# Kernel optimization log

Measured on AMD Instinct MI355X. Metric: run time of the kernel, lower is better.

Reference implementation:

```python
import jax, jax.numpy as jnp
import numpy as np

B, N, D_IN, D_OUT = 8, 2048, 1024, 1024


def setup_inputs() -> dict:
    key = jax.random.key(0)
    k0, k1, k2, k3 = jax.random.split(key, 4)
    scale = 1.0 / np.sqrt(D_IN)
    x = jax.random.normal(k0, (B, N, D_IN), dtype=jnp.float32)
    Wq = jax.random.normal(k1, (D_IN, D_OUT), dtype=jnp.float32) * scale
    Wk = jax.random.normal(k2, (D_IN, D_OUT), dtype=jnp.float32) * scale
    Wv = jax.random.normal(k3, (D_IN, D_OUT), dtype=jnp.float32) * scale
    return {"x": x, "Wq": Wq, "Wk": Wk, "Wv": Wv}


def reference(x, Wq, Wk, Wv):
    # x: [b, n, d_in]; single-head causal attention, dropout p=0 (eval).
    q = jnp.einsum('bnd,de->bne', x, Wq)
    k = jnp.einsum('bnd,de->bne', x, Wk)
    v = jnp.einsum('bnd,de->bne', x, Wv)
    n = x.shape[1]
    scores = jnp.einsum('bqe,bke->bqk', q, k)  # [b, n, n]
    causal_mask = jnp.triu(jnp.ones((n, n), dtype=bool), k=1)
    scores = jnp.where(causal_mask, -jnp.inf, scores)
    scale = 1.0 / jnp.sqrt(jnp.asarray(k.shape[-1], dtype=scores.dtype))
    attn = jax.nn.softmax(scores * scale, axis=-1)
    context = jnp.einsum('bqk,bke->bqe', attn, v)
    return context
```

## Files before the change

kernel.cpp:

```cpp
#include <hip/hip_runtime.h>


typedef unsigned short u16;
typedef __bf16 bf16x8 __attribute__((ext_vector_type(8)));
typedef float f32x4 __attribute__((ext_vector_type(4)));
typedef unsigned short u16x8 __attribute__((ext_vector_type(8)));
typedef unsigned short u16x4 __attribute__((ext_vector_type(4)));

static constexpr int BATCH = 8;
static constexpr int SEQ = 2048;
static constexpr int DIM = 1024;

static constexpr size_t SZ_XB = (size_t)BATCH * SEQ * DIM * 2;
static constexpr size_t SZ_W  = (size_t)DIM * DIM * 2;
static constexpr size_t OFF_XB  = 0;
static constexpr size_t OFF_WQT = OFF_XB + SZ_XB;
static constexpr size_t OFF_WKT = OFF_WQT + SZ_W;
static constexpr size_t OFF_WVT = OFF_WKT + SZ_W;
static constexpr size_t OFF_Q   = OFF_WVT + SZ_W;
static constexpr size_t OFF_K   = OFF_Q + SZ_XB;
static constexpr size_t OFF_VT  = OFF_K + SZ_XB;
static constexpr size_t OFF_E   = OFF_VT + SZ_XB;

__device__ __forceinline__ u16 f2b(float f) {
  unsigned u = __builtin_bit_cast(unsigned, f);
  u += 0x7fffu + ((u >> 16) & 1u);
  return (u16)(u >> 16);
}

__device__ __forceinline__ void gload16(const u16* g, u16* l) {
  __builtin_amdgcn_global_load_lds((__attribute__((address_space(1))) void*)g,
                                   (__attribute__((address_space(3))) void*)l, 16, 0, 0);
}

#define VWAIT(N) asm volatile("s_waitcnt vmcnt(" #N ")" ::: "memory")

__device__ __forceinline__ void barrier_raw() {
  __builtin_amdgcn_sched_barrier(0);
  __builtin_amdgcn_s_barrier();
  __builtin_amdgcn_sched_barrier(0);
}

__global__ __launch_bounds__(256) void cast_f32_bf16(const float* __restrict__ in,
                                                     u16* __restrict__ out) {
  const size_t i = ((size_t)blockIdx.x * 256 + threadIdx.x) * 8;
  float4 a = *(const float4*)(in + i);
  float4 b = *(const float4*)(in + i + 4);
  u16x8 o;
  o[0] = f2b(a.x); o[1] = f2b(a.y); o[2] = f2b(a.z); o[3] = f2b(a.w);
  o[4] = f2b(b.x); o[5] = f2b(b.y); o[6] = f2b(b.z); o[7] = f2b(b.w);
  *reinterpret_cast<u16x8*>(out + i) = o;
}

__global__ __launch_bounds__(256) void transpose_cast_w(const float* __restrict__ W,
                                                        u16* __restrict__ WT) {
  __shared__ float t[32][33];
  const int k0 = blockIdx.x * 32, n0 = blockIdx.y * 32;
  const int tx = threadIdx.x, ty = threadIdx.y;
#pragma unroll
  for (int dy = 0; dy < 32; dy += 8)
    t[ty + dy][tx] = W[(size_t)(k0 + ty + dy) * DIM + n0 + tx];
  __syncthreads();
#pragma unroll
  for (int dy = 0; dy < 32; dy += 8)
    WT[(size_t)(n0 + ty + dy) * DIM + k0 + tx] = f2b(t[tx][ty + dy]);
}

template <int MODE>
__global__ __launch_bounds__(512, 2) void gemm256(
    const u16* __restrict__ A, size_t sA, int lda,
    const u16* __restrict__ Bt, size_t sB, int ldb,
    void* __restrict__ C, size_t sC, int ldc,
    int Kdim, float scale) {
  const int bx = blockIdx.x, by = blockIdx.y, bz = blockIdx.z;
  if (MODE == 2 && bx > by) return;
  const u16* Ab = A + (size_t)bz * sA;
  const u16* Bb = Bt + (size_t)bz * sB;
  const int rowTile = by * 256, colTile = bx * 256;
  const int NT = Kdim >> 5;

  __shared__ __align__(16) u16 lds[4 * 16384];

  const int tid = threadIdx.x;
  const int w = tid >> 6, l = tid & 63;
  const int wm = w >> 2, wn = w & 3;
  const int lr = l & 15, quad = l >> 4;

  auto srow = [](int c) { int u = (c & 7) ^ ((c >> 3) & 7); return 2 * (c >> 3) + (u >> 2); };
  auto skq  = [](int c) { int u = (c & 7) ^ ((c >> 3) & 7); return u & 3; };
  const u16* pA0 = Ab + (size_t)(rowTile + srow(tid)) * lda + skq(tid) * 8;
  const u16* pA1 = Ab + (size_t)(rowTile + srow(tid + 512)) * lda + skq(tid + 512) * 8;
  const u16* pB0 = Bb + (size_t)(colTile + srow(tid)) * ldb + skq(tid) * 8;
  const u16* pB1 = Bb + (size_t)(colTile + srow(tid + 512)) * ldb + skq(tid + 512) * 8;

  int offA[8], offB[4];
#pragma unroll
  for (int mi = 0; mi < 8; ++mi) {
    const int row = wm * 128 + mi * 16 + lr;
    offA[mi] = ((row * 64 + quad * 16) ^ (((row >> 1) & 7) << 4)) >> 1;
  }
#pragma unroll
  for (int ni = 0; ni < 4; ++ni) {
    const int row = wn * 64 + ni * 16 + lr;
    offB[ni] = ((row * 64 + quad * 16) ^ (((row >> 1) & 7) << 4)) >> 1;
  }

  f32x4 acc[8][4];
#pragma unroll
  for (int i = 0; i < 8; ++i)
#pragma unroll
    for (int j = 0; j < 4; ++j) acc[i][j] = (f32x4){0.f, 0.f, 0.f, 0.f};

#define STAGE256(tt)                              \
  {                                               \
    u16* sb = &lds[((tt) & 3) * 16384];           \
    const int ko = (tt) * 32;                     \
    gload16(pA0 + ko, sb + w * 512);              \
    gload16(pA1 + ko, sb + 4096 + w * 512);       \
    gload16(pB0 + ko, sb + 8192 + w * 512);       \
    gload16(pB1 + ko, sb + 12288 + w * 512);      \
  }

  STAGE256(0);
  STAGE256(1);
  STAGE256(2);

  for (int t = 0; t < NT; ++t) {
    const u16* As = &lds[(t & 3) * 16384];
    const u16* Bs = As + 8192;
    if (t + 3 < NT) {
      STAGE256(t + 3);
      VWAIT(12);
    } else if (t + 2 < NT) {
      VWAIT(8);
    } else if (t + 1 < NT) {
      VWAIT(4);
    } else {
      VWAIT(0);
    }
    barrier_raw();
    bf16x8 af[8], bf[4];
#pragma unroll
    for (int mi = 0; mi < 8; ++mi)
      af[mi] = *reinterpret_cast<const bf16x8*>(&As[offA[mi]]);
#pragma unroll
    for (int ni = 0; ni < 4; ++ni)
      bf[ni] = *reinterpret_cast<const bf16x8*>(&Bs[offB[ni]]);
    __builtin_amdgcn_s_setprio(1);
#pragma unroll
    for (int mi = 0; mi < 8; ++mi)
#pragma unroll
      for (int ni = 0; ni < 4; ++ni)
        acc[mi][ni] =
            __builtin_amdgcn_mfma_f32_16x16x32_bf16(af[mi], bf[ni], acc[mi][ni], 0, 0, 0);
    __builtin_amdgcn_s_setprio(0);
    asm volatile("s_waitcnt lgkmcnt(0)" ::: "memory");
    barrier_raw();
  }
#undef STAGE256

  const int orow0 = rowTile + wm * 128 + quad * 4;
  const int ocol0 = colTile + wn * 64 + lr;
#pragma unroll
  for (int mi = 0; mi < 8; ++mi) {
#pragma unroll
    for (int ni = 0; ni < 4; ++ni) {
      const int colg = ocol0 + ni * 16;
      if (MODE == 1) {
        const int rowg0 = orow0 + mi * 16;
        const int bb = rowg0 >> 11, nn = rowg0 & (SEQ - 1);
        u16x4 pk;
#pragma unroll
        for (int r = 0; r < 4; ++r) pk[r] = f2b(acc[mi][ni][r]);
        *reinterpret_cast<u16x4*>(&((u16*)C)[(size_t)bb * sC + (size_t)colg * ldc + nn]) = pk;
      } else {
#pragma unroll
        for (int r = 0; r < 4; ++r) {
          const int rowg = orow0 + mi * 16 + r;
          const float v = acc[mi][ni][r];
          if (MODE == 0) {
            ((u16*)C)[(size_t)bz * sC + (size_t)rowg * ldc + colg] = f2b(v);
          } else {
            const float e = (colg <= rowg) ? __expf(v * scale) : 0.f;
            ((u16*)C)[(size_t)bz * sC + (size_t)rowg * ldc + colg] = f2b(e);
          }
        }
      }
    }
  }
}

template <int MODE>
__global__ __launch_bounds__(256, 2) void gemm_bt(
    const u16* __restrict__ A, size_t sA, int lda,
    const u16* __restrict__ Bt, size_t sB, int ldb,
    void* __restrict__ C, size_t sC, int ldc,
    int Kdim, float scale) {
  const int bx = blockIdx.x, bz = blockIdx.z;
  const int by = (MODE == 3) ? (int)(gridDim.y - 1 - blockIdx.y) : (int)blockIdx.y;
  if (MODE == 2 && bx > by) return;
  const u16* Ab = A + (size_t)bz * sA;
  const u16* Bb = Bt + (size_t)bz * sB;
  const int rowTile = by * 128, colTile = bx * 128;
  int kmax = Kdim;
  if (MODE == 3) {
    int km = (by + 1) * 128;
    if (km < kmax) kmax = km;
  }

  __shared__ __align__(16) u16 As[128 * 32];
  __shared__ __align__(16) u16 Bs[128 * 32];

  const int tid = threadIdx.x;
  const int w = tid >> 6, l = tid & 63;
  const int wr = (w >> 1) * 64, wc = (w & 1) * 64;
  const int lr = l & 15, quad = l >> 4;

  f32x4 acc[4][4];
#pragma unroll
  for (int i = 0; i < 4; ++i)
#pragma unroll
    for (int j = 0; j < 4; ++j) acc[i][j] = (f32x4){0.f, 0.f, 0.f, 0.f};
  float rsum[4] = {0.f, 0.f, 0.f, 0.f};

  const int srow = w * 16 + (l >> 2);
  const int scol = (l & 3) * 8;
  const u16* gA0 = Ab + (size_t)(rowTile + srow) * lda + scol;
  const u16* gA1 = gA0 + (size_t)64 * lda;
  const u16* gB0 = Bb + (size_t)(colTile + srow) * ldb + scol;
  const u16* gB1 = gB0 + (size_t)64 * ldb;
  u16* lA0 = &As[(w * 16) * 32];
  u16* lA1 = &As[(64 + w * 16) * 32];
  u16* lB0 = &Bs[(w * 16) * 32];
  u16* lB1 = &Bs[(64 + w * 16) * 32];

  for (int k0 = 0; k0 < kmax; k0 += 32) {
    __syncthreads();
    gload16(gA0 + k0, lA0);
    gload16(gA1 + k0, lA1);
    gload16(gB0 + k0, lB0);
    gload16(gB1 + k0, lB1);
    __syncthreads();
    bf16x8 af[4], bfr[4];
#pragma unroll
    for (int mi = 0; mi < 4; ++mi)
      af[mi] = *reinterpret_cast<const bf16x8*>(&As[(wr + mi * 16 + lr) * 32 + quad * 8]);
#pragma unroll
    for (int ni = 0; ni < 4; ++ni)
      bfr[ni] = *reinterpret_cast<const bf16x8*>(&Bs[(wc + ni * 16 + lr) * 32 + quad * 8]);
    if (MODE == 3) {
#pragma unroll
      for (int mi = 0; mi < 4; ++mi) {
        float s = 0.f;
#pragma unroll
        for (int j = 0; j < 8; ++j) s += (float)af[mi][j];
        rsum[mi] += s;
      }
    }
#pragma unroll
    for (int mi = 0; mi < 4; ++mi)
#pragma unroll
      for (int ni = 0; ni < 4; ++ni)
        acc[mi][ni] =
            __builtin_amdgcn_mfma_f32_16x16x32_bf16(af[mi], bfr[ni], acc[mi][ni], 0, 0, 0);
  }

  if (MODE == 3) {
#pragma unroll
    for (int mi = 0; mi < 4; ++mi) {
      rsum[mi] += __shfl_xor(rsum[mi], 16);
      rsum[mi] += __shfl_xor(rsum[mi], 32);
    }
  }

  const int orow0 = rowTile + wr + quad * 4;
  const int ocol0 = colTile + wc + lr;
#pragma unroll
  for (int mi = 0; mi < 4; ++mi) {
    float linv[4];
    if (MODE == 3) {
#pragma unroll
      for (int r = 0; r < 4; ++r) linv[r] = 1.f / __shfl(rsum[mi], quad * 4 + r);
    }
#pragma unroll
    for (int ni = 0; ni < 4; ++ni) {
      const int colg = ocol0 + ni * 16;
#pragma unroll
      for (int r = 0; r < 4; ++r) {
        const int rowg = orow0 + mi * 16 + r;
        const float v = acc[mi][ni][r];
        if (MODE == 0) {
          ((u16*)C)[(size_t)bz * sC + (size_t)rowg * ldc + colg] = f2b(v);
        } else if (MODE == 1) {
          const int bb = rowg >> 11, nn = rowg & (SEQ - 1);
          ((u16*)C)[(size_t)bb * sC + (size_t)colg * ldc + nn] = f2b(v);
        } else if (MODE == 2) {
          const float e = (colg <= rowg) ? __expf(v * scale) : 0.f;
          ((u16*)C)[(size_t)bz * sC + (size_t)rowg * ldc + colg] = f2b(e);
        } else {
          ((float*)C)[(size_t)bz * sC + (size_t)rowg * ldc + colg] = v * linv[r];
        }
      }
    }
  }
}

extern "C" void kernel_launch(void* const* d_in, const int* in_sizes, int n_in,
                              void* d_out, int out_size, void* d_ws, size_t ws_size,
                              hipStream_t stream) {
  const float* x = (const float*)d_in[0];
  const float* Wq = (const float*)d_in[1];
  const float* Wk = (const float*)d_in[2];
  const float* Wv = (const float*)d_in[3];
  float* out = (float*)d_out;
  char* ws = (char*)d_ws;

  u16* xb = (u16*)(ws + OFF_XB);
  u16* wqT = (u16*)(ws + OFF_WQT);
  u16* wkT = (u16*)(ws + OFF_WKT);
  u16* wvT = (u16*)(ws + OFF_WVT);
  u16* qb = (u16*)(ws + OFF_Q);
  u16* kb = (u16*)(ws + OFF_K);
  u16* vt = (u16*)(ws + OFF_VT);
  u16* eb = (u16*)(ws + OFF_E);

  const int total = BATCH * SEQ * DIM;
  cast_f32_bf16<<<total / (256 * 8), 256, 0, stream>>>(x, xb);
  transpose_cast_w<<<dim3(32, 32), dim3(32, 8), 0, stream>>>(Wq, wqT);
  transpose_cast_w<<<dim3(32, 32), dim3(32, 8), 0, stream>>>(Wk, wkT);
  transpose_cast_w<<<dim3(32, 32), dim3(32, 8), 0, stream>>>(Wv, wvT);

  gemm256<0><<<dim3(4, 64, 1), 512, 0, stream>>>(xb, 0, DIM, wqT, 0, DIM, qb, 0, DIM,
                                                 DIM, 1.f);
  gemm256<0><<<dim3(4, 64, 1), 512, 0, stream>>>(xb, 0, DIM, wkT, 0, DIM, kb, 0, DIM,
                                                 DIM, 1.f);
  gemm256<1><<<dim3(4, 64, 1), 512, 0, stream>>>(xb, 0, DIM, wvT, 0, DIM, vt,
                                                 (size_t)DIM * SEQ, SEQ, DIM, 1.f);
  gemm256<2><<<dim3(8, 8, BATCH), 512, 0, stream>>>(
      qb, (size_t)SEQ * DIM, DIM, kb, (size_t)SEQ * DIM, DIM, eb, (size_t)SEQ * SEQ, SEQ,
      DIM, 0.03125f);
  gemm_bt<3><<<dim3(8, 16, BATCH), 256, 0, stream>>>(
      eb, (size_t)SEQ * SEQ, SEQ, vt, (size_t)DIM * SEQ, SEQ, out, (size_t)SEQ * DIM, DIM,
      SEQ, 1.f);
}
```

Baseline: 417.4 us.

## Run PV GEMM on 256-tile pipelined kernel and split main loop into half-steps

Removes the simple 128-tile gemm_bt kernel. The attention-times-V GEMM now runs through the 256x256 four-stage LDS-pipelined kernel, with causal K truncation, row-sum accumulation and normalization added to it. The main loop is also restructured for all modes: B and A tile loads are issued separately, and the MFMA work is split into two halves so the LDS reads and next-stage loads for the second half overlap the first half's compute. The goal is better latency hiding and data reuse in the largest GEMM. The cost is more barriers per iteration, and bigger tiles leave fewer blocks with coarser causal work balance.

```diff
diff --git a/kernel.cpp b/kernel.cpp
--- a/kernel.cpp
+++ b/kernel.cpp
@@ -72,12 +72,18 @@
     const u16* __restrict__ Bt, size_t sB, int ldb,
     void* __restrict__ C, size_t sC, int ldc,
     int Kdim, float scale) {
-  const int bx = blockIdx.x, by = blockIdx.y, bz = blockIdx.z;
+  const int bx = blockIdx.x, bz = blockIdx.z;
+  const int by = (MODE == 3) ? (int)(gridDim.y - 1 - blockIdx.y) : (int)blockIdx.y;
   if (MODE == 2 && bx > by) return;
   const u16* Ab = A + (size_t)bz * sA;
   const u16* Bb = Bt + (size_t)bz * sB;
   const int rowTile = by * 256, colTile = bx * 256;
-  const int NT = Kdim >> 5;
+  int kmax = Kdim;
+  if (MODE == 3) {
+    int km = (by + 1) * 256;
+    if (km < kmax) kmax = km;
+  }
+  const int NT = kmax >> 5;
 
   __shared__ __align__(16) u16 lds[4 * 16384];
 
@@ -110,59 +116,110 @@
   for (int i = 0; i < 8; ++i)
 #pragma unroll
     for (int j = 0; j < 4; ++j) acc[i][j] = (f32x4){0.f, 0.f, 0.f, 0.f};
-
-#define STAGE256(tt)                              \
+  float rsum[8] = {0.f, 0.f, 0.f, 0.f, 0.f, 0.f, 0.f, 0.f};
+
+#define STAGE_B(tt)                               \
+  {                                               \
+    u16* sb = &lds[((tt) & 3) * 16384];           \
+    const int ko = (tt) * 32;                     \
+    gload16(pB0 + ko, sb + 8192 + w * 512);       \
+    gload16(pB1 + ko, sb + 12288 + w * 512);      \
+  }
+#define STAGE_A(tt)                               \
   {                                               \
     u16* sb = &lds[((tt) & 3) * 16384];           \
     const int ko = (tt) * 32;                     \
     gload16(pA0 + ko, sb + w * 512);              \
     gload16(pA1 + ko, sb + 4096 + w * 512);       \
-    gload16(pB0 + ko, sb + 8192 + w * 512);       \
-    gload16(pB1 + ko, sb + 12288 + w * 512);      \
-  }
-
-  STAGE256(0);
-  STAGE256(1);
-  STAGE256(2);
+  }
+
+  STAGE_B(0); STAGE_A(0);
+  STAGE_B(1); STAGE_A(1);
+  STAGE_B(2); STAGE_A(2);
+  VWAIT(8);
+  barrier_raw();
 
   for (int t = 0; t < NT; ++t) {
     const u16* As = &lds[(t & 3) * 16384];
     const u16* Bs = As + 8192;
-    if (t + 3 < NT) {
-      STAGE256(t + 3);
-      VWAIT(12);
-    } else if (t + 2 < NT) {
-      VWAIT(8);
-    } else if (t + 1 < NT) {
-      VWAIT(4);
-    } else {
-      VWAIT(0);
-    }
-    barrier_raw();
     bf16x8 af[8], bf[4];
-#pragma unroll
-    for (int mi = 0; mi < 8; ++mi)
+
+#pragma unroll
+    for (int mi = 0; mi < 4; ++mi)
       af[mi] = *reinterpret_cast<const bf16x8*>(&As[offA[mi]]);
 #pragma unroll
     for (int ni = 0; ni < 4; ++ni)
       bf[ni] = *reinterpret_cast<const bf16x8*>(&Bs[offB[ni]]);
+    if (t + 3 < NT) STAGE_B(t + 3);
+    barrier_raw();
+    if (MODE == 3) {
+#pragma unroll
+      for (int mi = 0; mi < 4; ++mi) {
+        float s = 0.f;
+#pragma unroll
+        for (int j = 0; j < 8; ++j) s += (float)af[mi][j];
+        rsum[mi] += s;
+      }
+    }
     __builtin_amdgcn_s_setprio(1);
 #pragma unroll
-    for (int mi = 0; mi < 8; ++mi)
+    for (int mi = 0; mi < 4; ++mi)
 #pragma unroll
       for (int ni = 0; ni < 4; ++ni)
         acc[mi][ni] =
             __builtin_amdgcn_mfma_f32_16x16x32_bf16(af[mi], bf[ni], acc[mi][ni], 0, 0, 0);
     __builtin_amdgcn_s_setprio(0);
-    asm volatile("s_waitcnt lgkmcnt(0)" ::: "memory");
+
+#pragma unroll
+    for (int mi = 4; mi < 8; ++mi)
+      af[mi] = *reinterpret_cast<const bf16x8*>(&As[offA[mi]]);
+    if (t + 3 < NT) {
+      STAGE_A(t + 3);
+      VWAIT(8);
+    } else if (t + 2 < NT) {
+      VWAIT(4);
+    } else if (t + 1 < NT) {
+      VWAIT(0);
+    }
     barrier_raw();
-  }
-#undef STAGE256
+    if (MODE == 3) {
+#pragma unroll
+      for (int mi = 4; mi < 8; ++mi) {
+        float s = 0.f;
+#pragma unroll
+        for (int j = 0; j < 8; ++j) s += (float)af[mi][j];
+        rsum[mi] += s;
+      }
+    }
+    __builtin_amdgcn_s_setprio(1);
+#pragma unroll
+    for (int mi = 4; mi < 8; ++mi)
+#pragma unroll
+      for (int ni = 0; ni < 4; ++ni)
+        acc[mi][ni] =
+            __builtin_amdgcn_mfma_f32_16x16x32_bf16(af[mi], bf[ni], acc[mi][ni], 0, 0, 0);
+    __builtin_amdgcn_s_setprio(0);
+  }
+#undef STAGE_A
+#undef STAGE_B
+
+  if (MODE == 3) {
+#pragma unroll
+    for (int mi = 0; mi < 8; ++mi) {
+      rsum[mi] += __shfl_xor(rsum[mi], 16);
+      rsum[mi] += __shfl_xor(rsum[mi], 32);
+    }
+  }
 
   const int orow0 = rowTile + wm * 128 + quad * 4;
   const int ocol0 = colTile + wn * 64 + lr;
 #pragma unroll
   for (int mi = 0; mi < 8; ++mi) {
+    float linv[4];
+    if (MODE == 3) {
+#pragma unroll
+      for (int r = 0; r < 4; ++r) linv[r] = 1.f / __shfl(rsum[mi], quad * 4 + r);
+    }
 #pragma unroll
     for (int ni = 0; ni < 4; ++ni) {
       const int colg = ocol0 + ni * 16;
@@ -180,125 +237,12 @@
           const float v = acc[mi][ni][r];
           if (MODE == 0) {
             ((u16*)C)[(size_t)bz * sC + (size_t)rowg * ldc + colg] = f2b(v);
-          } else {
+          } else if (MODE == 2) {
             const float e = (colg <= rowg) ? __expf(v * scale) : 0.f;
             ((u16*)C)[(size_t)bz * sC + (size_t)rowg * ldc + colg] = f2b(e);
+          } else {
+            ((float*)C)[(size_t)bz * sC + (size_t)rowg * ldc + colg] = v * linv[r];
           }
-        }
-      }
-    }
-  }
-}
-
-template <int MODE>
-__global__ __launch_bounds__(256, 2) void gemm_bt(
-    const u16* __restrict__ A, size_t sA, int lda,
-    const u16* __restrict__ Bt, size_t sB, int ldb,
-    void* __restrict__ C, size_t sC, int ldc,
-    int Kdim, float scale) {
-  const int bx = blockIdx.x, bz = blockIdx.z;
-  const int by = (MODE == 3) ? (int)(gridDim.y - 1 - blockIdx.y) : (int)blockIdx.y;
-  if (MODE == 2 && bx > by) return;
-  const u16* Ab = A + (size_t)bz * sA;
-  const u16* Bb = Bt + (size_t)bz * sB;
-  const int rowTile = by * 128, colTile = bx * 128;
-  int kmax = Kdim;
-  if (MODE == 3) {
-    int km = (by + 1) * 128;
-    if (km < kmax) kmax = km;
-  }
-
-  __shared__ __align__(16) u16 As[128 * 32];
-  __shared__ __align__(16) u16 Bs[128 * 32];
-
-  const int tid = threadIdx.x;
-  const int w = tid >> 6, l = tid & 63;
-  const int wr = (w >> 1) * 64, wc = (w & 1) * 64;
-  const int lr = l & 15, quad = l >> 4;
-
-  f32x4 acc[4][4];
-#pragma unroll
-  for (int i = 0; i < 4; ++i)
-#pragma unroll
-    for (int j = 0; j < 4; ++j) acc[i][j] = (f32x4){0.f, 0.f, 0.f, 0.f};
-  float rsum[4] = {0.f, 0.f, 0.f, 0.f};
-
-  const int srow = w * 16 + (l >> 2);
-  const int scol = (l & 3) * 8;
-  const u16* gA0 = Ab + (size_t)(rowTile + srow) * lda + scol;
-  const u16* gA1 = gA0 + (size_t)64 * lda;
-  const u16* gB0 = Bb + (size_t)(colTile + srow) * ldb + scol;
-  const u16* gB1 = gB0 + (size_t)64 * ldb;
-  u16* lA0 = &As[(w * 16) * 32];
-  u16* lA1 = &As[(64 + w * 16) * 32];
-  u16* lB0 = &Bs[(w * 16) * 32];
-  u16* lB1 = &Bs[(64 + w * 16) * 32];
-
-  for (int k0 = 0; k0 < kmax; k0 += 32) {
-    __syncthreads();
-    gload16(gA0 + k0, lA0);
-    gload16(gA1 + k0, lA1);
-    gload16(gB0 + k0, lB0);
-    gload16(gB1 + k0, lB1);
-    __syncthreads();
-    bf16x8 af[4], bfr[4];
-#pragma unroll
-    for (int mi = 0; mi < 4; ++mi)
-      af[mi] = *reinterpret_cast<const bf16x8*>(&As[(wr + mi * 16 + lr) * 32 + quad * 8]);
-#pragma unroll
-    for (int ni = 0; ni < 4; ++ni)
-      bfr[ni] = *reinterpret_cast<const bf16x8*>(&Bs[(wc + ni * 16 + lr) * 32 + quad * 8]);
-    if (MODE == 3) {
-#pragma unroll
-      for (int mi = 0; mi < 4; ++mi) {
-        float s = 0.f;
-#pragma unroll
-        for (int j = 0; j < 8; ++j) s += (float)af[mi][j];
-        rsum[mi] += s;
-      }
-    }
-#pragma unroll
-    for (int mi = 0; mi < 4; ++mi)
-#pragma unroll
-      for (int ni = 0; ni < 4; ++ni)
-        acc[mi][ni] =
-            __builtin_amdgcn_mfma_f32_16x16x32_bf16(af[mi], bfr[ni], acc[mi][ni], 0, 0, 0);
-  }
-
-  if (MODE == 3) {
-#pragma unroll
-    for (int mi = 0; mi < 4; ++mi) {
-      rsum[mi] += __shfl_xor(rsum[mi], 16);
-      rsum[mi] += __shfl_xor(rsum[mi], 32);
-    }
-  }
-
-  const int orow0 = rowTile + wr + quad * 4;
-  const int ocol0 = colTile + wc + lr;
-#pragma unroll
-  for (int mi = 0; mi < 4; ++mi) {
-    float linv[4];
-    if (MODE == 3) {
-#pragma unroll
-      for (int r = 0; r < 4; ++r) linv[r] = 1.f / __shfl(rsum[mi], quad * 4 + r);
-    }
-#pragma unroll
-    for (int ni = 0; ni < 4; ++ni) {
-      const int colg = ocol0 + ni * 16;
-#pragma unroll
-      for (int r = 0; r < 4; ++r) {
-        const int rowg = orow0 + mi * 16 + r;
-        const float v = acc[mi][ni][r];
-        if (MODE == 0) {
-          ((u16*)C)[(size_t)bz * sC + (size_t)rowg * ldc + colg] = f2b(v);
-        } else if (MODE == 1) {
-          const int bb = rowg >> 11, nn = rowg & (SEQ - 1);
-          ((u16*)C)[(size_t)bb * sC + (size_t)colg * ldc + nn] = f2b(v);
-        } else if (MODE == 2) {
-          const float e = (colg <= rowg) ? __expf(v * scale) : 0.f;
-          ((u16*)C)[(size_t)bz * sC + (size_t)rowg * ldc + colg] = f2b(e);
-        } else {
-          ((float*)C)[(size_t)bz * sC + (size_t)rowg * ldc + colg] = v * linv[r];
         }
       }
     }
@@ -339,7 +283,7 @@
   gemm256<2><<<dim3(8, 8, BATCH), 512, 0, stream>>>(
       qb, (size_t)SEQ * DIM, DIM, kb, (size_t)SEQ * DIM, DIM, eb, (size_t)SEQ * SEQ, SEQ,
       DIM, 0.03125f);
-  gemm_bt<3><<<dim3(8, 16, BATCH), 256, 0, stream>>>(
+  gemm256<3><<<dim3(4, 8, BATCH), 512, 0, stream>>>(
       eb, (size_t)SEQ * SEQ, SEQ, vt, (size_t)DIM * SEQ, SEQ, out, (size_t)SEQ * DIM, DIM,
       SEQ, 1.f);
 }
```

New measurement: 391.3 us. 6.2% less time.
